# Optimization experiments

Measured on AMD Instinct MI355X. Metric: run time of the kernel, lower is better.

The kernel has to match this reference:

```python
import jax, jax.numpy as jnp
import numpy as np

B, L, D = 8, 2048, 1024
FF_MULT = 2
EPS = 1e-6


def _layernorm(x):
    # elementwise_affine=False, eps=1e-6
    mu = jnp.mean(x, axis=-1, keepdims=True)
    var = jnp.mean(jnp.square(x - mu), axis=-1, keepdims=True)
    return (x - mu) / jnp.sqrt(var + EPS)


def setup_inputs() -> dict:
    key = jax.random.key(0)
    ks = jax.random.split(key, 20)
    s = 0.02
    inp = {
        "x": jax.random.normal(ks[0], (B, L, D), jnp.float32),
        "t": jax.random.normal(ks[1], (B, D), jnp.float32),
        "mask": jax.random.randint(ks[2], (B, L), 0, 2) > 0,
        # AdaLayerNormSimple.linear: dim -> 3*dim
        "ada_w": jax.random.normal(ks[3], (D, 3 * D), jnp.float32) * s,
        "ada_b": jnp.zeros((3 * D,), jnp.float32),
        # forward SSM (fallback: Linear->GELU->Linear)
        "ssm_w1": jax.random.normal(ks[4], (D, D), jnp.float32) * s,
        "ssm_b1": jnp.zeros((D,), jnp.float32),
        "ssm_w2": jax.random.normal(ks[5], (D, D), jnp.float32) * s,
        "ssm_b2": jnp.zeros((D,), jnp.float32),
        # backward SSM (independent weights)
        "bwd_w1": jax.random.normal(ks[6], (D, D), jnp.float32) * s,
        "bwd_b1": jnp.zeros((D,), jnp.float32),
        "bwd_w2": jax.random.normal(ks[7], (D, D), jnp.float32) * s,
        "bwd_b2": jnp.zeros((D,), jnp.float32),
        # ff_ada_proj: dim -> 3*dim
        "ffada_w": jax.random.normal(ks[8], (D, 3 * D), jnp.float32) * s,
        "ffada_b": jnp.zeros((3 * D,), jnp.float32),
        # FeedForward: dim -> 2*dim -> dim, gelu(tanh)
        "ff_w1": jax.random.normal(ks[9], (D, FF_MULT * D), jnp.float32) * s,
        "ff_b1": jnp.zeros((FF_MULT * D,), jnp.float32),
        "ff_w2": jax.random.normal(ks[10], (FF_MULT * D, D), jnp.float32) * s,
        "ff_b2": jnp.zeros((D,), jnp.float32),
    }
    return inp


def _ssm_fallback(u, w1, b1, w2, b2):
    # _FallbackMamba3: Linear -> GELU(exact) -> Dropout(identity, p=0) -> Linear
    h = jax.nn.gelu(u @ w1 + b1, approximate=False)
    return h @ w2 + b2


def reference(x, t, mask, ada_w, ada_b, ssm_w1, ssm_b1, ssm_w2, ssm_b2,
              bwd_w1, bwd_b1, bwd_w2, bwd_b2, ffada_w, ffada_b,
              ff_w1, ff_b1, ff_w2, ff_b2):
    m = mask[:, :, None]  # [B, L, 1]

    # --- AdaLayerNormSimple ---
    emb = jax.nn.silu(t) @ ada_w + ada_b            # [B, 3D]
    shift, scale, gate_msa = jnp.split(emb, 3, axis=1)
    norm = _layernorm(x) * (1.0 + scale[:, None]) + shift[:, None]
    norm = jnp.where(m, norm, 0.0)

    # --- bidirectional SSM (fallback impl) ---
    fwd = _ssm_fallback(norm, ssm_w1, ssm_b1, ssm_w2, ssm_b2)
    bwd = jnp.flip(_ssm_fallback(jnp.flip(norm, axis=1), bwd_w1, bwd_b1, bwd_w2, bwd_b2), axis=1)
    ssm_out = jnp.where(m, fwd + bwd, 0.0)
    x = x + gate_msa[:, None] * ssm_out

    # --- AdaLN-conditioned FeedForward ---
    ff_ada = jax.nn.silu(t) @ ffada_w + ffada_b     # [B, 3D]
    shift_mlp, scale_mlp, gate_mlp = jnp.split(ff_ada, 3, axis=1)
    ff_norm = _layernorm(x) * (1.0 + scale_mlp[:, None]) + shift_mlp[:, None]
    h = jax.nn.gelu(ff_norm @ ff_w1 + ff_b1, approximate=True)  # approximate='tanh'
    ff_out = h @ ff_w2 + ff_b2
    return x + gate_mlp[:, None] * ff_out
```

## Files before the change

### kernel.cpp

```cpp
#include <hip/hip_runtime.h>
#include <hip/hip_bf16.h>

namespace {

constexpr int D_      = 1024;
constexpr int THREE_D = 3072;
constexpr int B_      = 8;
constexpr int M_      = 16384;

typedef unsigned short u16;
typedef __attribute__((ext_vector_type(8))) short bf16x8;
typedef __attribute__((ext_vector_type(4))) float f32x4;

__device__ __forceinline__ u16 f2bf(float f) {
  unsigned u = __float_as_uint(f);
  u += 0x7fffu + ((u >> 16) & 1u);
  return (u16)(u >> 16);
}

__device__ __forceinline__ float gelu_fast(float x) {
  float u = 0.7978845608028654f * (x + 0.044715f * x * x * x);
  float e = __expf(2.0f * u);
  float th = 1.0f - 2.0f * __builtin_amdgcn_rcpf(e + 1.0f);
  return 0.5f * x * (1.0f + th);
}

typedef __attribute__((address_space(3))) unsigned int   lds_uint;
typedef const __attribute__((address_space(1))) unsigned int gl_uint;
__device__ __forceinline__ void gload16(const void* g, void* l) {
  __builtin_amdgcn_global_load_lds((gl_uint*)g, (lds_uint*)l, 16, 0, 0);
}

typedef __attribute__((address_space(3))) const u16 lds_cu16;
__device__ __forceinline__ bf16x8 ds_read128(const u16* p) {
  bf16x8 r;
  asm volatile("ds_read_b128 %0, %1" : "=v"(r) : "v"((lds_cu16*)p));
  return r;
}

#define BAR() asm volatile("s_barrier" ::: "memory")
#define LGKM0() do { asm volatile("s_waitcnt lgkmcnt(0)" ::: "memory"); \
                     __builtin_amdgcn_sched_barrier(0); } while (0)

__global__ void packT(const float* __restrict__ s0, const float* __restrict__ s1,
                      u16* __restrict__ dst, int K, int N, int mode) {
  __shared__ float tile[32][33];
  int n0 = blockIdx.x * 32, k0 = blockIdx.y * 32;
  int tx = threadIdx.x, ty = threadIdx.y;
  for (int i = ty; i < 32; i += 8) {
    int k = k0 + i, n = n0 + tx;
    float v;
    if (mode == 1)      { int h = N >> 1; v = (n < h) ? s0[(size_t)k * h + n] : s1[(size_t)k * h + (n - h)]; }
    else if (mode == 2) { int h = K >> 1; v = (k < h) ? s0[(size_t)k * N + n] : s1[(size_t)(k - h) * N + n]; }
    else                v = s0[(size_t)k * N + n];
    tile[i][tx] = v;
  }
  __syncthreads();
  for (int i = ty; i < 32; i += 8) {
    int n = n0 + i, k = k0 + tx;
    dst[(size_t)n * K + k] = f2bf(tile[tx][i]);
  }
}

__global__ __launch_bounds__(256) void ada_part(const float* __restrict__ t,
                                                const float* __restrict__ W,
                                                float* __restrict__ part) {
  __shared__ float s[B_ * 256];
  const int jb = blockIdx.x, kc = blockIdx.y;
  const int tid = threadIdx.x;
  const int k0 = kc * 256;
  for (int idx = tid; idx < B_ * 256; idx += 256) {
    float v = t[((idx >> 8) << 10) + k0 + (idx & 255)];
    s[idx] = v / (1.0f + expf(-v));
  }
  __syncthreads();
  const int j = jb * 256 + tid;
  float acc[B_];
#pragma unroll
  for (int b = 0; b < B_; ++b) acc[b] = 0.f;
  for (int k = 0; k < 256; ++k) {
    const float w = W[(size_t)(k0 + k) * THREE_D + j];
#pragma unroll
    for (int b = 0; b < B_; ++b) acc[b] = fmaf(s[(b << 8) + k], w, acc[b]);
  }
#pragma unroll
  for (int b = 0; b < B_; ++b)
    part[((size_t)kc * B_ + b) * THREE_D + j] = acc[b];
}

__global__ __launch_bounds__(256) void ada_reduce(const float* __restrict__ part,
                                                  const float* __restrict__ bias,
                                                  float* __restrict__ out) {
  const int j = blockIdx.x * 256 + threadIdx.x;
  const int b = blockIdx.y;
  float v = bias[j];
#pragma unroll
  for (int kc = 0; kc < 4; ++kc) v += part[((size_t)kc * B_ + b) * THREE_D + j];
  out[(size_t)b * THREE_D + j] = v;
}

__global__ __launch_bounds__(256) void compact_mask(const int* __restrict__ mask,
                                                    int* __restrict__ cnt,
                                                    int* __restrict__ cidx) {
  const int m = blockIdx.x * 256 + threadIdx.x;
  if (mask[m] != 0) {
    int p = atomicAdd(cnt, 1);
    cidx[p] = m;
  }
}

__global__ __launch_bounds__(256) void pad_tail(const int* __restrict__ cnt,
                                                int* __restrict__ cidx,
                                                u16* __restrict__ normc,
                                                int* __restrict__ mpad) {
  const int c = *cnt;
  const int pad = (c + 255) & ~255;
  if (blockIdx.x == 0 && threadIdx.x == 0) *mpad = pad;
  const int p = c + blockIdx.x;
  if (p < pad) {
    if (threadIdx.x == 0) cidx[p] = -1;
    ((uint2*)(normc + (size_t)p * D_))[threadIdx.x] = (uint2){0u, 0u};
  }
}

__global__ __launch_bounds__(256) void copy_unmasked(const float* __restrict__ x,
                                                     const int* __restrict__ mask,
                                                     float* __restrict__ out) {
  const int row = blockIdx.x;
  if (mask[row] != 0) return;
  const int tid = threadIdx.x;
  *(float4*)(out + (size_t)row * D_ + tid * 4) =
      *(const float4*)(x + (size_t)row * D_ + tid * 4);
}

__global__ __launch_bounds__(256) void ln_mod(const float* __restrict__ in,
                                              const float* __restrict__ modv,
                                              u16* __restrict__ out) {
  const int row = blockIdx.x;
  const int b = row >> 11;
  const int tid = threadIdx.x;
  const float4 v = *(const float4*)(in + (size_t)row * D_ + tid * 4);
  float s = v.x + v.y + v.z + v.w;
  float q = v.x * v.x + v.y * v.y + v.z * v.z + v.w * v.w;
#pragma unroll
  for (int off = 32; off > 0; off >>= 1) {
    s += __shfl_down(s, off);
    q += __shfl_down(q, off);
  }
  __shared__ float red[8];
  const int wave = tid >> 6, lane = tid & 63;
  if (lane == 0) { red[wave] = s; red[4 + wave] = q; }
  __syncthreads();
  float ts = red[0] + red[1] + red[2] + red[3];
  float tq = red[4] + red[5] + red[6] + red[7];
  const float mu = ts * (1.0f / D_);
  const float var = tq * (1.0f / D_) - mu * mu;
  const float rstd = rsqrtf(var + 1e-6f);
  const float4 sh = *(const float4*)(modv + (size_t)b * THREE_D + tid * 4);
  const float4 sc = *(const float4*)(modv + (size_t)b * THREE_D + D_ + tid * 4);
  float o0 = (v.x - mu) * rstd * (1.0f + sc.x) + sh.x;
  float o1 = (v.y - mu) * rstd * (1.0f + sc.y) + sh.y;
  float o2 = (v.z - mu) * rstd * (1.0f + sc.z) + sh.z;
  float o3 = (v.w - mu) * rstd * (1.0f + sc.w) + sh.w;
  uint2 pk;
  pk.x = (unsigned)f2bf(o0) | ((unsigned)f2bf(o1) << 16);
  pk.y = (unsigned)f2bf(o2) | ((unsigned)f2bf(o3) << 16);
  *(uint2*)(out + (size_t)row * D_ + tid * 4) = pk;
}

__global__ __launch_bounds__(256) void ln_mod_idx(const float* __restrict__ in,
                                                  const float* __restrict__ modv,
                                                  const int* __restrict__ cnt,
                                                  const int* __restrict__ cidx,
                                                  u16* __restrict__ out) {
  const int p = blockIdx.x;
  if (p >= *cnt) return;
  const int row = cidx[p];
  const int b = row >> 11;
  const int tid = threadIdx.x;
  const float4 v = *(const float4*)(in + (size_t)row * D_ + tid * 4);
  float s = v.x + v.y + v.z + v.w;
  float q = v.x * v.x + v.y * v.y + v.z * v.z + v.w * v.w;
#pragma unroll
  for (int off = 32; off > 0; off >>= 1) {
    s += __shfl_down(s, off);
    q += __shfl_down(q, off);
  }
  __shared__ float red[8];
  const int wave = tid >> 6, lane = tid & 63;
  if (lane == 0) { red[wave] = s; red[4 + wave] = q; }
  __syncthreads();
  float ts = red[0] + red[1] + red[2] + red[3];
  float tq = red[4] + red[5] + red[6] + red[7];
  const float mu = ts * (1.0f / D_);
  const float var = tq * (1.0f / D_) - mu * mu;
  const float rstd = rsqrtf(var + 1e-6f);
  const float4 sh = *(const float4*)(modv + (size_t)b * THREE_D + tid * 4);
  const float4 sc = *(const float4*)(modv + (size_t)b * THREE_D + D_ + tid * 4);
  float o0 = (v.x - mu) * rstd * (1.0f + sc.x) + sh.x;
  float o1 = (v.y - mu) * rstd * (1.0f + sc.y) + sh.y;
  float o2 = (v.z - mu) * rstd * (1.0f + sc.z) + sh.z;
  float o3 = (v.w - mu) * rstd * (1.0f + sc.w) + sh.w;
  uint2 pk;
  pk.x = (unsigned)f2bf(o0) | ((unsigned)f2bf(o1) << 16);
  pk.y = (unsigned)f2bf(o2) | ((unsigned)f2bf(o3) << 16);
  *(uint2*)(out + (size_t)p * D_ + tid * 4) = pk;
}

constexpr int BM = 256, BN = 256, BK = 64;

template <int EPI, int NN, int KK>
__global__ __launch_bounds__(512, 2)
void gemm_bt(const u16* __restrict__ A, const u16* __restrict__ Bt,
             const float* __restrict__ b0, const float* __restrict__ b1,
             const float* __restrict__ xres, const int* __restrict__ cidx,
             const int* __restrict__ mpad,
             const float* __restrict__ gate,
             float* __restrict__ outf, u16* __restrict__ outh) {
  __shared__ u16 As[2][BM * BK];
  __shared__ u16 Bs[2][BN * BK];
  const int tid = threadIdx.x;
  const int wave = tid >> 6, lane = tid & 63;
  const int wr = wave >> 2, wc = wave & 3;
  const int l15 = lane & 15, l4 = lane >> 4;

  constexpr int LGX = (NN == 2048) ? 3 : 2;
  const int nwg = gridDim.x;
  const int flat = blockIdx.x;
  int bx, by;
  if constexpr (EPI == 0 || EPI == 2) {
    constexpr int NBY = M_ / BM;
    by = flat % NBY;
    bx = flat / NBY;
  } else {
    const int swz = (flat & 7) * (nwg >> 3) + (flat >> 3);
    bx = swz & ((1 << LGX) - 1);
    by = swz >> LGX;
  }
  const int m0 = by * BM, n0 = bx * BN;

  if constexpr (EPI == 0 || EPI == 2) {
    if (m0 >= *mpad) return;
  }

  const int sg = (lane & 7) ^ (lane >> 3);
  const int srow = wave * 8 + (lane >> 3);
  const u16* ga = A  + (size_t)(m0 + srow) * KK + sg * 8;
  const u16* gb = Bt + (size_t)(n0 + srow) * KK + sg * 8;
  const int ldq = wave * 8 * BK;

  const int swz0 = ((l4 ^ (l15 & 7)) << 3);
  const int swz1 = (((4 + l4) ^ (l15 & 7)) << 3);
  const int arow = (wr * 128 + l15) * BK;
  const int brow = (wc * 64 + l15) * BK;

  f32x4 acc[8][4];
#pragma unroll
  for (int i = 0; i < 8; ++i)
#pragma unroll
    for (int j = 0; j < 4; ++j) acc[i][j] = (f32x4){0.f, 0.f, 0.f, 0.f};

  constexpr int NT = KK / BK;

#define STG_A(q, dst, gp) gload16((gp) + (size_t)((q) * 64) * KK, (dst) + ((q) * 64) * BK + ldq)
#define STG_B(q, dst, gp) gload16((gp) + (size_t)((q) * 64) * KK, (dst) + ((q) * 64) * BK + ldq)

  STG_B(0, Bs[0], gb); STG_B(1, Bs[0], gb); STG_B(2, Bs[0], gb); STG_B(3, Bs[0], gb);
  STG_A(0, As[0], ga); STG_A(2, As[0], ga);
  STG_A(1, As[0], ga); STG_A(3, As[0], ga);
  asm volatile("s_waitcnt vmcnt(2)" ::: "memory");
  BAR();

  const u16* gan = ga + BK;
  const u16* gbn = gb + BK;

  bf16x8 af0[4], af1[4], bf0[4], bf1[4];
  for (int t = 0; t < NT; ++t) {
    const u16* as = As[t & 1];
    const u16* bs = Bs[t & 1];
    u16* An = As[(t + 1) & 1];
    u16* Bn = Bs[(t + 1) & 1];
    const bool pre = (t + 1 < NT);

#pragma unroll
    for (int i = 0; i < 4; ++i) af0[i] = ds_read128(as + arow + i * 16 * BK + swz0);
#pragma unroll
    for (int j = 0; j < 4; ++j) bf0[j] = ds_read128(bs + brow + j * 16 * BK + swz0);
    if (pre) { STG_B(0, Bn, gbn); STG_B(1, Bn, gbn); STG_B(2, Bn, gbn); STG_B(3, Bn, gbn); }
    LGKM0();
    __builtin_amdgcn_s_setprio(1);
#pragma unroll
    for (int i = 0; i < 4; ++i)
#pragma unroll
      for (int j = 0; j < 4; ++j)
        acc[i][j] = __builtin_amdgcn_mfma_f32_16x16x32_bf16(af0[i], bf0[j], acc[i][j], 0, 0, 0);
    __builtin_amdgcn_s_setprio(0);

#pragma unroll
    for (int i = 0; i < 4; ++i) af1[i] = ds_read128(as + arow + i * 16 * BK + swz1);
#pragma unroll
    for (int j = 0; j < 4; ++j) bf1[j] = ds_read128(bs + brow + j * 16 * BK + swz1);
    if (pre) {
      STG_A(0, An, gan); STG_A(2, An, gan);
      asm volatile("s_waitcnt vmcnt(6)" ::: "memory");
    } else {
      asm volatile("s_waitcnt vmcnt(0)" ::: "memory");
    }
    BAR();
    LGKM0();
    __builtin_amdgcn_s_setprio(1);
#pragma unroll
    for (int i = 0; i < 4; ++i)
#pragma unroll
      for (int j = 0; j < 4; ++j)
        acc[i][j] = __builtin_amdgcn_mfma_f32_16x16x32_bf16(af1[i], bf1[j], acc[i][j], 0, 0, 0);
    __builtin_amdgcn_s_setprio(0);

#pragma unroll
    for (int i = 0; i < 4; ++i) af0[i] = ds_read128(as + arow + (64 + i * 16) * BK + swz0);
    if (pre) { STG_A(1, An, gan); STG_A(3, An, gan); }
    LGKM0();
    __builtin_amdgcn_s_setprio(1);
#pragma unroll
    for (int i = 0; i < 4; ++i)
#pragma unroll
      for (int j = 0; j < 4; ++j)
        acc[4 + i][j] = __builtin_amdgcn_mfma_f32_16x16x32_bf16(af0[i], bf0[j], acc[4 + i][j], 0, 0, 0);
    __builtin_amdgcn_s_setprio(0);

#pragma unroll
    for (int i = 0; i < 4; ++i) af1[i] = ds_read128(as + arow + (64 + i * 16) * BK + swz1);
    if (pre) asm volatile("s_waitcnt vmcnt(2)" ::: "memory");
    BAR();
    LGKM0();
    __builtin_amdgcn_s_setprio(1);
#pragma unroll
    for (int i = 0; i < 4; ++i)
#pragma unroll
      for (int j = 0; j < 4; ++j)
        acc[4 + i][j] = __builtin_amdgcn_mfma_f32_16x16x32_bf16(af1[i], bf1[j], acc[4 + i][j], 0, 0, 0);
    __builtin_amdgcn_s_setprio(0);

    gan += BK; gbn += BK;
  }
#undef STG_A
#undef STG_B

#pragma unroll
  for (int i = 0; i < 8; ++i) {
#pragma unroll
    for (int r = 0; r < 4; ++r) {
      const int m = m0 + wr * 128 + i * 16 + l4 * 4 + r;
      int row = m;
      if constexpr (EPI == 2) {
        row = cidx[m];
        if (row < 0) continue;
      }
#pragma unroll
      for (int j = 0; j < 4; ++j) {
        const int n = n0 + wc * 64 + j * 16 + l15;
        float v = acc[i][j][r];
        if constexpr (EPI == 0 || EPI == 1) {
          v += (n < (NN >> 1)) ? b0[n] : b1[n - (NN >> 1)];
          outh[(size_t)m * NN + n] = f2bf(gelu_fast(v));
        } else if constexpr (EPI == 2) {
          v += b0[n] + b1[n];
          outf[(size_t)row * NN + n] = xres[(size_t)row * NN + n] +
                                       gate[(size_t)(row >> 11) * THREE_D + n] * v;
        } else {
          v += b0[n];
          outf[(size_t)m * NN + n] = outf[(size_t)m * NN + n] +
                                     gate[(size_t)(m >> 11) * THREE_D + n] * v;
        }
      }
    }
  }
}

}

extern "C" void kernel_launch(void* const* d_in, const int* in_sizes, int n_in,
                              void* d_out, int out_size, void* d_ws, size_t ws_size,
                              hipStream_t stream) {
  const float* x       = (const float*)d_in[0];
  const float* t       = (const float*)d_in[1];
  const int*   mask    = (const int*)d_in[2];
  const float* ada_w   = (const float*)d_in[3];
  const float* ada_b   = (const float*)d_in[4];
  const float* ssm_w1  = (const float*)d_in[5];
  const float* ssm_b1  = (const float*)d_in[6];
  const float* ssm_w2  = (const float*)d_in[7];
  const float* ssm_b2  = (const float*)d_in[8];
  const float* bwd_w1  = (const float*)d_in[9];
  const float* bwd_b1  = (const float*)d_in[10];
  const float* bwd_w2  = (const float*)d_in[11];
  const float* bwd_b2  = (const float*)d_in[12];
  const float* ffada_w = (const float*)d_in[13];
  const float* ffada_b = (const float*)d_in[14];
  const float* ff_w1   = (const float*)d_in[15];
  const float* ff_b1   = (const float*)d_in[16];
  const float* ff_w2   = (const float*)d_in[17];
  const float* ff_b2   = (const float*)d_in[18];
  float* out = (float*)d_out;

  char* ws = (char*)d_ws;
  u16* normb = (u16*)ws;
  u16* Hb    = (u16*)(ws + (size_t)M_ * D_ * 2);
  u16* w1t   = (u16*)(ws + (size_t)M_ * D_ * 2 + (size_t)M_ * 2 * D_ * 2);
  u16* w2t   = w1t + (size_t)2 * D_ * D_;
  u16* fw1t  = w2t + (size_t)2 * D_ * D_;
  u16* fw2t  = fw1t + (size_t)2 * D_ * D_;
  float* emb   = (float*)(fw2t + (size_t)2 * D_ * D_);
  float* ffada = emb + B_ * THREE_D;
  int* cnt   = (int*)(ffada + B_ * THREE_D);
  int* mpad  = cnt + 1;
  int* cidx  = mpad + 7;
  float* part0 = (float*)Hb;
  float* part1 = part0 + 4 * B_ * THREE_D;

  dim3 tb(32, 8);
  packT<<<dim3(64, 32), tb, 0, stream>>>(ssm_w1, bwd_w1, w1t, D_, 2 * D_, 1);
  packT<<<dim3(32, 64), tb, 0, stream>>>(ssm_w2, bwd_w2, w2t, 2 * D_, D_, 2);
  packT<<<dim3(64, 32), tb, 0, stream>>>(ff_w1, nullptr, fw1t, D_, 2 * D_, 0);
  packT<<<dim3(32, 64), tb, 0, stream>>>(ff_w2, nullptr, fw2t, 2 * D_, D_, 0);

  ada_part<<<dim3(12, 4), 256, 0, stream>>>(t, ada_w, part0);
  ada_part<<<dim3(12, 4), 256, 0, stream>>>(t, ffada_w, part1);
  ada_reduce<<<dim3(12, 8), 256, 0, stream>>>(part0, ada_b, emb);
  ada_reduce<<<dim3(12, 8), 256, 0, stream>>>(part1, ffada_b, ffada);

  hipMemsetAsync(cnt, 0, sizeof(int), stream);
  compact_mask<<<64, 256, 0, stream>>>(mask, cnt, cidx);
  pad_tail<<<256, 256, 0, stream>>>(cnt, cidx, normb, mpad);
  copy_unmasked<<<M_, 256, 0, stream>>>(x, mask, out);
  ln_mod_idx<<<M_, 256, 0, stream>>>(x, emb, cnt, cidx, normb);

  gemm_bt<0, 2048, 1024><<<512, 512, 0, stream>>>(normb, w1t,
                                                  ssm_b1, bwd_b1, nullptr, nullptr, mpad, nullptr,
                                                  nullptr, Hb);
  gemm_bt<2, 1024, 2048><<<256, 512, 0, stream>>>(Hb, w2t,
                                                  ssm_b2, bwd_b2, x, cidx, mpad, emb + 2 * D_,
                                                  out, nullptr);
  ln_mod<<<M_, 256, 0, stream>>>(out, ffada, normb);
  gemm_bt<1, 2048, 1024><<<512, 512, 0, stream>>>(normb, fw1t,
                                                  ff_b1, ff_b1 + D_, nullptr, nullptr, nullptr, nullptr,
                                                  nullptr, Hb);
  gemm_bt<3, 1024, 2048><<<256, 512, 0, stream>>>(Hb, fw2t,
                                                  ff_b2, nullptr, nullptr, nullptr, nullptr, ffada + 2 * D_,
                                                  out, nullptr);
}
```

Baseline: 394.9 us.

## Split SSM second GEMM along K into two bf16 partials plus combine kernel

The second SSM GEMM (K=2048, 256 tiles) is split into two K-halves, giving 512 workgroups that each write a bf16 partial sum. A new combine2 kernel then adds the two partials, the biases and the gated residual, and scatters rows back through the compaction index. This targets low occupancy from only 256 workgroups on a 256-CU device. In exchange it adds extra partial-buffer traffic, one more launch, and rounds the partial sums to bf16 before they are added.

```diff
diff --git a/kernel.cpp b/kernel.cpp
--- a/kernel.cpp
+++ b/kernel.cpp
@@ -16,6 +16,9 @@
   unsigned u = __float_as_uint(f);
   u += 0x7fffu + ((u >> 16) & 1u);
   return (u16)(u >> 16);
+}
+__device__ __forceinline__ float bf2f(u16 h) {
+  return __uint_as_float(((unsigned)h) << 16);
 }
 
 __device__ __forceinline__ float gelu_fast(float x) {
@@ -131,6 +134,32 @@
   const int tid = threadIdx.x;
   *(float4*)(out + (size_t)row * D_ + tid * 4) =
       *(const float4*)(x + (size_t)row * D_ + tid * 4);
+}
+
+__global__ __launch_bounds__(256) void combine2(const u16* __restrict__ p0,
+                                                const u16* __restrict__ p1,
+                                                const float* __restrict__ x,
+                                                const int* __restrict__ mpad,
+                                                const int* __restrict__ cidx,
+                                                const float* __restrict__ b0,
+                                                const float* __restrict__ b1,
+                                                const float* __restrict__ gate,
+                                                float* __restrict__ out) {
+  const int p = blockIdx.x;
+  if (p >= *mpad) return;
+  const int row = cidx[p];
+  if (row < 0) return;
+  const int j = threadIdx.x * 4;
+  const uint2 a = *(const uint2*)(p0 + (size_t)p * D_ + j);
+  const uint2 b = *(const uint2*)(p1 + (size_t)p * D_ + j);
+  const float4 xv = *(const float4*)(x + (size_t)row * D_ + j);
+  const float* gp = gate + (size_t)(row >> 11) * THREE_D + j;
+  float4 o;
+  o.x = xv.x + gp[0] * (bf2f((u16)(a.x & 0xffff)) + bf2f((u16)(b.x & 0xffff)) + b0[j]     + b1[j]);
+  o.y = xv.y + gp[1] * (bf2f((u16)(a.x >> 16))    + bf2f((u16)(b.x >> 16))    + b0[j + 1] + b1[j + 1]);
+  o.z = xv.z + gp[2] * (bf2f((u16)(a.y & 0xffff)) + bf2f((u16)(b.y & 0xffff)) + b0[j + 2] + b1[j + 2]);
+  o.w = xv.w + gp[3] * (bf2f((u16)(a.y >> 16))    + bf2f((u16)(b.y >> 16))    + b0[j + 3] + b1[j + 3]);
+  *(float4*)(out + (size_t)row * D_ + j) = o;
 }
 
 __global__ __launch_bounds__(256) void ln_mod(const float* __restrict__ in,
@@ -213,10 +242,10 @@
 __global__ __launch_bounds__(512, 2)
 void gemm_bt(const u16* __restrict__ A, const u16* __restrict__ Bt,
              const float* __restrict__ b0, const float* __restrict__ b1,
-             const float* __restrict__ xres, const int* __restrict__ cidx,
              const int* __restrict__ mpad,
              const float* __restrict__ gate,
-             float* __restrict__ outf, u16* __restrict__ outh) {
+             float* __restrict__ outf, u16* __restrict__ outh,
+             u16* __restrict__ outh2) {
   __shared__ u16 As[2][BM * BK];
   __shared__ u16 Bs[2][BN * BK];
   const int tid = threadIdx.x;
@@ -227,8 +256,12 @@
   constexpr int LGX = (NN == 2048) ? 3 : 2;
   const int nwg = gridDim.x;
   const int flat = blockIdx.x;
-  int bx, by;
-  if constexpr (EPI == 0 || EPI == 2) {
+  int bx, by, ks = 0;
+  if constexpr (EPI == 4) {
+    by = flat & 63;
+    bx = (flat >> 6) & 3;
+    ks = flat >> 8;
+  } else if constexpr (EPI == 0) {
     constexpr int NBY = M_ / BM;
     by = flat % NBY;
     bx = flat / NBY;
@@ -239,14 +272,14 @@
   }
   const int m0 = by * BM, n0 = bx * BN;
 
-  if constexpr (EPI == 0 || EPI == 2) {
+  if constexpr (EPI == 0 || EPI == 4) {
     if (m0 >= *mpad) return;
   }
 
   const int sg = (lane & 7) ^ (lane >> 3);
   const int srow = wave * 8 + (lane >> 3);
-  const u16* ga = A  + (size_t)(m0 + srow) * KK + sg * 8;
-  const u16* gb = Bt + (size_t)(n0 + srow) * KK + sg * 8;
+  const u16* ga = A  + (size_t)(m0 + srow) * KK + ks * 1024 + sg * 8;
+  const u16* gb = Bt + (size_t)(n0 + srow) * KK + ks * 1024 + sg * 8;
   const int ldq = wave * 8 * BK;
 
   const int swz0 = ((l4 ^ (l15 & 7)) << 3);
@@ -260,7 +293,7 @@
 #pragma unroll
     for (int j = 0; j < 4; ++j) acc[i][j] = (f32x4){0.f, 0.f, 0.f, 0.f};
 
-  constexpr int NT = KK / BK;
+  constexpr int NT = (EPI == 4) ? 16 : KK / BK;
 
 #define STG_A(q, dst, gp) gload16((gp) + (size_t)((q) * 64) * KK, (dst) + ((q) * 64) * BK + ldq)
 #define STG_B(q, dst, gp) gload16((gp) + (size_t)((q) * 64) * KK, (dst) + ((q) * 64) * BK + ldq)
@@ -346,16 +379,14 @@
 #undef STG_A
 #undef STG_B
 
+  u16* ph = nullptr;
+  if constexpr (EPI == 4) ph = (ks == 0) ? outh : outh2;
+
 #pragma unroll
   for (int i = 0; i < 8; ++i) {
 #pragma unroll
     for (int r = 0; r < 4; ++r) {
       const int m = m0 + wr * 128 + i * 16 + l4 * 4 + r;
-      int row = m;
-      if constexpr (EPI == 2) {
-        row = cidx[m];
-        if (row < 0) continue;
-      }
 #pragma unroll
       for (int j = 0; j < 4; ++j) {
         const int n = n0 + wc * 64 + j * 16 + l15;
@@ -363,10 +394,8 @@
         if constexpr (EPI == 0 || EPI == 1) {
           v += (n < (NN >> 1)) ? b0[n] : b1[n - (NN >> 1)];
           outh[(size_t)m * NN + n] = f2bf(gelu_fast(v));
-        } else if constexpr (EPI == 2) {
-          v += b0[n] + b1[n];
-          outf[(size_t)row * NN + n] = xres[(size_t)row * NN + n] +
-                                       gate[(size_t)(row >> 11) * THREE_D + n] * v;
+        } else if constexpr (EPI == 4) {
+          ph[(size_t)m * NN + n] = f2bf(v);
         } else {
           v += b0[n];
           outf[(size_t)m * NN + n] = outf[(size_t)m * NN + n] +
@@ -415,6 +444,8 @@
   int* cnt   = (int*)(ffada + B_ * THREE_D);
   int* mpad  = cnt + 1;
   int* cidx  = mpad + 7;
+  u16* p1    = (u16*)(cidx + M_);
+  u16* p0    = normb;
   float* part0 = (float*)Hb;
   float* part1 = part0 + 4 * B_ * THREE_D;
 
@@ -436,16 +467,19 @@
   ln_mod_idx<<<M_, 256, 0, stream>>>(x, emb, cnt, cidx, normb);
 
   gemm_bt<0, 2048, 1024><<<512, 512, 0, stream>>>(normb, w1t,
-                                                  ssm_b1, bwd_b1, nullptr, nullptr, mpad, nullptr,
-                                                  nullptr, Hb);
-  gemm_bt<2, 1024, 2048><<<256, 512, 0, stream>>>(Hb, w2t,
-                                                  ssm_b2, bwd_b2, x, cidx, mpad, emb + 2 * D_,
-                                                  out, nullptr);
+                                                  ssm_b1, bwd_b1, mpad, nullptr,
+                                                  nullptr, Hb, nullptr);
+  gemm_bt<4, 1024, 2048><<<512, 512, 0, stream>>>(Hb, w2t,
+                                                  nullptr, nullptr, mpad, nullptr,
+                                                  nullptr, p0, p1);
+  combine2<<<M_, 256, 0, stream>>>(p0, p1, x, mpad, cidx, ssm_b2, bwd_b2,
+                                   emb + 2 * D_, out);
+
   ln_mod<<<M_, 256, 0, stream>>>(out, ffada, normb);
   gemm_bt<1, 2048, 1024><<<512, 512, 0, stream>>>(normb, fw1t,
-                                                  ff_b1, ff_b1 + D_, nullptr, nullptr, nullptr, nullptr,
-                                                  nullptr, Hb);
+                                                  ff_b1, ff_b1 + D_, nullptr, nullptr,
+                                                  nullptr, Hb, nullptr);
   gemm_bt<3, 1024, 2048><<<256, 512, 0, stream>>>(Hb, fw2t,
-                                                  ff_b2, nullptr, nullptr, nullptr, nullptr, ffada + 2 * D_,
-                                                  out, nullptr);
-}
+                                                  ff_b2, nullptr, nullptr, ffada + 2 * D_,
+                                                  out, nullptr, nullptr);
+}
```

After: 382.2 us. 1.03x faster.
